# Performance work log

Measured on AMD Instinct MI355X. Metric: run time of the kernel, lower is better.

The kernel has to match this reference:

```python
import jax, jax.numpy as jnp
import numpy as np

B, T = 4096, 256
COND, INTV, H = 128, 64, 256


def _glorot(key, shape):
    fan_in = shape[0]
    return jax.random.normal(key, shape, dtype=jnp.float32) / np.sqrt(fan_in)


def setup_inputs() -> dict:
    key = jax.random.key(0)
    ks = jax.random.split(key, 20)
    inp = {
        "cond": jax.random.normal(ks[0], (B, COND), dtype=jnp.float32),
        "interval_feat": jax.random.normal(ks[1], (B, INTV), dtype=jnp.float32),
        "times": jnp.cumsum(jax.random.uniform(ks[2], (B, T), dtype=jnp.float32), axis=1),
        "seq_lens": jax.random.randint(ks[3], (B,), 1, T + 1),
        # seq_feature MLP: INTV -> 2*INTV -> 2*INTV -> INTV
        "w1": _glorot(ks[4], (INTV, 2 * INTV)), "b1": jnp.zeros((2 * INTV,), jnp.float32),
        "w2": _glorot(ks[5], (2 * INTV, 2 * INTV)), "b2": jnp.zeros((2 * INTV,), jnp.float32),
        "w3": _glorot(ks[6], (2 * INTV, INTV)), "b3": jnp.zeros((INTV,), jnp.float32),
        # h0 projection: (COND+INTV) -> H
        "w_h0": _glorot(ks[7], (COND + INTV, H)), "b_h0": jnp.zeros((H,), jnp.float32),
        # GRUCell (input dim 1), gate order r,z,n
        "w_ih": _glorot(ks[8], (1, 3 * H)), "b_ih": jnp.zeros((3 * H,), jnp.float32),
        "w_hh": _glorot(ks[9], (H, 3 * H)), "b_hh": jnp.zeros((3 * H,), jnp.float32),
        # head: H -> 2 (delta, stop logit)
        "w_head": _glorot(ks[10], (H, 2)), "b_head": jnp.zeros((2,), jnp.float32),
    }
    return inp


def reference(cond, interval_feat, times, seq_lens,
              w1, b1, w2, b2, w3, b3, w_h0, b_h0,
              w_ih, w_hh, b_ih, b_hh, w_head, b_head):
    # seq_feature MLP
    s = jax.nn.relu(interval_feat @ w1 + b1)
    s = jax.nn.relu(s @ w2 + b2)
    seq_emb = s @ w3 + b3
    # initial hidden state
    h0 = jnp.tanh(jnp.concatenate([cond, seq_emb], axis=-1) @ w_h0 + b_h0)  # (B,H)
    # ground-truth deltas; step 0 input is 0, step i>=1 input is gt_delta[:, i-1]
    gt_delta = jnp.diff(times, axis=1, prepend=jnp.zeros((times.shape[0], 1), times.dtype))  # (B,T)
    xs = jnp.concatenate([jnp.zeros((1, times.shape[0]), times.dtype), gt_delta.T], axis=0)  # (T+1,B)

    def step(h, x):
        gi = x[:, None] * w_ih[0] + b_ih          # (B,3H)
        gh = h @ w_hh + b_hh                       # (B,3H)
        gi_r, gi_z, gi_n = jnp.split(gi, 3, axis=-1)
        gh_r, gh_z, gh_n = jnp.split(gh, 3, axis=-1)
        r = jax.nn.sigmoid(gi_r + gh_r)
        z = jax.nn.sigmoid(gi_z + gh_z)
        n = jnp.tanh(gi_n + r * gh_n)
        h_new = (1.0 - z) * n + z * h
        out = h_new @ w_head + b_head              # (B,2)
        return h_new, out

    _, outs = jax.lax.scan(step, h0, xs)           # outs: (T+1,B,2)
    pred_delta = outs[:, :, 0].T                   # (B,T+1)
    stop_logits = outs[:, :, 1].T                  # (B,T+1)
    return pred_delta, stop_logits
```

## Files before the change

kernel.cpp:

```cpp
#include <hip/hip_runtime.h>
#include <cstddef>

typedef _Float16 f16x8 __attribute__((ext_vector_type(8)));
typedef _Float16 f16x2 __attribute__((ext_vector_type(2)));
typedef float    f32x4 __attribute__((ext_vector_type(4)));

#define Bc 4096
#define Tc 256
#define NSTEP 257
#define RB 16
#define HSTR 264
#define GSTR 12
#define HEAD_OFF 393216

__device__ inline float sigm(float x)  { return __builtin_amdgcn_rcpf(1.f + __expf(-x)); }
__device__ inline float tanh_(float x) { return 1.f - 2.f * __builtin_amdgcn_rcpf(1.f + __expf(2.f * x)); }

__global__ __launch_bounds__(256) void build_frags(
    const float* __restrict__ w_hh, const float* __restrict__ w_head,
    _Float16* __restrict__ ws)
{
    int flat = blockIdx.x * 256 + threadIdx.x;
    if (blockIdx.x < 96) {
        int f    = flat >> 6;
        int lane = flat & 63;
        int kt   = f & 7;
        int nc   = (f >> 3) % 3;
        int trio = f / 24;
        int c     = nc * 256 + (trio >> 1) * 32 + 2 * (lane & 15) + (trio & 1);
        int kbase = kt * 32 + (lane >> 4) * 8;
        _Float16* dst = ws + (size_t)f * 512 + (size_t)lane * 8;
        #pragma unroll
        for (int j = 0; j < 8; ++j)
            dst[j] = (_Float16)w_hh[(size_t)(kbase + j) * 768 + c];
    } else {
        int idx = flat - 96 * 256;
        int kt   = idx >> 6;
        int lane = idx & 63;
        int col   = lane & 15;
        int kbase = kt * 32 + (lane >> 4) * 8;
        _Float16* dst = ws + HEAD_OFF / 2 + (size_t)kt * 512 + (size_t)lane * 8;
        #pragma unroll
        for (int j = 0; j < 8; ++j)
            dst[j] = (col < 2) ? (_Float16)w_head[(size_t)(kbase + j) * 2 + col]
                               : (_Float16)0.f;
    }
}

__global__ __attribute__((amdgpu_waves_per_eu(2, 2))) __launch_bounds__(512)
void gru_mfma(
    const float* __restrict__ cond, const float* __restrict__ ivf,
    const float* __restrict__ times,
    const float* __restrict__ w1, const float* __restrict__ b1,
    const float* __restrict__ w2, const float* __restrict__ b2,
    const float* __restrict__ w3, const float* __restrict__ b3,
    const float* __restrict__ wh0, const float* __restrict__ bh0,
    const float* __restrict__ w_ih, const float* __restrict__ b_ih,
    const float* __restrict__ b_hh, const float* __restrict__ b_head,
    const _Float16* __restrict__ wfrag,
    float* __restrict__ out)
{
    __shared__ __align__(16) _Float16 h16[RB * HSTR];
    __shared__ __align__(16) float xs4[4 * NSTEP * 4];
    __shared__ __align__(16) _Float16 headB[4096];
    __shared__ __align__(16) float gateC[256 * GSTR];
    __shared__ float  outbuf[2][2][RB][16];
    __shared__ float  bh2[2];
    __shared__ float  mlp1[RB * 128];
    __shared__ float  mlp2[RB * 128];
    __shared__ float  embS[RB * 64];
    __shared__ float  h0f[RB * 256];

    const int tid  = threadIdx.x;
    const int w    = tid >> 6;
    const int lane = tid & 63;
    const int l15  = lane & 15;
    const int q    = lane >> 4;
    const int row0 = blockIdx.x * RB;

    for (int o = tid; o < RB * 128; o += 512) {
        int r = o >> 7, c = o & 127;
        float a = b1[c];
        #pragma unroll 4
        for (int k = 0; k < 64; ++k)
            a = fmaf(ivf[(size_t)(row0 + r) * 64 + k], w1[k * 128 + c], a);
        mlp1[o] = fmaxf(a, 0.f);
    }
    __syncthreads();
    for (int o = tid; o < RB * 128; o += 512) {
        int r = o >> 7, c = o & 127;
        float a = b2[c];
        #pragma unroll 4
        for (int k = 0; k < 128; ++k)
            a = fmaf(mlp1[r * 128 + k], w2[k * 128 + c], a);
        mlp2[o] = fmaxf(a, 0.f);
    }
    __syncthreads();
    for (int o = tid; o < RB * 64; o += 512) {
        int r = o >> 6, c = o & 63;
        float a = b3[c];
        #pragma unroll 4
        for (int k = 0; k < 128; ++k)
            a = fmaf(mlp2[r * 128 + k], w3[k * 64 + c], a);
        embS[o] = a;
    }
    __syncthreads();
    for (int o = tid; o < RB * 256; o += 512) {
        int r = o >> 8, c = o & 255;
        float a = bh0[c];
        #pragma unroll 4
        for (int k = 0; k < 128; ++k)
            a = fmaf(cond[(size_t)(row0 + r) * 128 + k], wh0[k * 256 + c], a);
        #pragma unroll 4
        for (int k = 0; k < 64; ++k)
            a = fmaf(embS[r * 64 + k], wh0[(128 + k) * 256 + c], a);
        float h = tanh_(a);
        h0f[o] = h;
        h16[r * HSTR + c] = (_Float16)h;
    }

    for (int o = tid; o < 4 * NSTEP; o += 512) {
        int qg = o / NSTEP, ii = o - qg * NSTEP;
        #pragma unroll
        for (int jj = 0; jj < 4; ++jj) {
            int r = qg * 4 + jj;
            float x = 0.f;
            if (ii >= 1) {
                float a = times[(size_t)(row0 + r) * Tc + (ii - 1)];
                float b = (ii >= 2) ? times[(size_t)(row0 + r) * Tc + (ii - 2)] : 0.f;
                x = a - b;
            }
            xs4[o * 4 + jj] = x;
        }
    }
    {
        const float4* src = (const float4*)(wfrag + HEAD_OFF / 2);
        ((float4*)headB)[tid] = src[tid];
    }
    for (int uu = tid; uu < 256; uu += 512) {
        gateC[uu * GSTR + 0] = w_ih[uu];
        gateC[uu * GSTR + 1] = w_ih[256 + uu];
        gateC[uu * GSTR + 2] = w_ih[512 + uu];
        gateC[uu * GSTR + 3] = b_ih[uu] + b_hh[uu];
        gateC[uu * GSTR + 4] = b_ih[256 + uu] + b_hh[256 + uu];
        gateC[uu * GSTR + 5] = b_ih[512 + uu];
        gateC[uu * GSTR + 6] = b_hh[512 + uu];
        gateC[uu * GSTR + 7] = 0.f;
    }
    if (tid < 2) bh2[tid] = b_head[tid];

    const int u0 = w * 32 + 2 * l15;
    const int u1 = u0 + 1;

    f16x8 Bf[2][3][8];
    #pragma unroll
    for (int p = 0; p < 2; ++p)
        #pragma unroll
        for (int nc = 0; nc < 3; ++nc)
            #pragma unroll
            for (int kt = 0; kt < 8; ++kt)
                Bf[p][nc][kt] = *(const f16x8*)(wfrag
                    + (size_t)(((2 * w + p) * 3 + nc) * 8 + kt) * 512
                    + (size_t)lane * 8);

    __syncthreads();

    float hold[2][4];
    #pragma unroll
    for (int p = 0; p < 2; ++p)
        #pragma unroll
        for (int j = 0; j < 4; ++j)
            hold[p][j] = h0f[(q * 4 + j) * 256 + u0 + p];

    for (int i = 0; i <= NSTEP; ++i) {
        const bool doGh = (i < NSTEP);
        const bool doHd = (i >= 1) && (w == 0);

        if (i >= 17 && ((i - 17) & 15) == 0) {
            const int obase = i - 17;
            const int par   = (obase >> 4) & 1;
            const int e     = tid & 15;
            const int row   = (tid >> 4) & 15;
            const int plane = tid >> 8;
            out[(size_t)plane * ((size_t)Bc * NSTEP)
                + (size_t)(row0 + row) * NSTEP + obase + e]
                = outbuf[par][plane][row][e] + bh2[plane];
        }

        f32x4 aR[2], aZ[2], aN[2];
        #pragma unroll
        for (int p = 0; p < 2; ++p) {
            aR[p] = (f32x4){0.f, 0.f, 0.f, 0.f};
            aZ[p] = (f32x4){0.f, 0.f, 0.f, 0.f};
            aN[p] = (f32x4){0.f, 0.f, 0.f, 0.f};
        }
        f32x4 aH = (f32x4){0.f, 0.f, 0.f, 0.f};

        const _Float16* abase = h16 + l15 * HSTR + q * 8;
        #pragma unroll
        for (int kt = 0; kt < 8; ++kt) {
            if (doGh || doHd) {
                f16x8 Af = *(const f16x8*)(abase + kt * 32);
                if (doGh) {
                    #pragma unroll
                    for (int p = 0; p < 2; ++p) {
                        aR[p] = __builtin_amdgcn_mfma_f32_16x16x32_f16(Af, Bf[p][0][kt], aR[p], 0, 0, 0);
                        aZ[p] = __builtin_amdgcn_mfma_f32_16x16x32_f16(Af, Bf[p][1][kt], aZ[p], 0, 0, 0);
                        aN[p] = __builtin_amdgcn_mfma_f32_16x16x32_f16(Af, Bf[p][2][kt], aN[p], 0, 0, 0);
                    }
                }
                if (doHd) {
                    f16x8 Bh = *(const f16x8*)(headB + kt * 512 + lane * 8);
                    aH = __builtin_amdgcn_mfma_f32_16x16x32_f16(Af, Bh, aH, 0, 0, 0);
                }
            }
        }

        if (doHd && l15 < 2) {
            const int o = i - 1;
            #pragma unroll
            for (int j = 0; j < 4; ++j)
                outbuf[(o >> 4) & 1][l15][q * 4 + j][o & 15] = aH[j];
        }

        __syncthreads();

        if (doGh) {
            const f32x4 xv  = *(const f32x4*)(xs4 + (q * NSTEP + i) * 4);
            const f32x4 g0a = *(const f32x4*)(gateC + u0 * GSTR);
            const f32x4 g1a = *(const f32x4*)(gateC + u0 * GSTR + 4);
            const f32x4 g0b = *(const f32x4*)(gateC + u1 * GSTR);
            const f32x4 g1b = *(const f32x4*)(gateC + u1 * GSTR + 4);
            #pragma unroll
            for (int j = 0; j < 4; ++j) {
                const int m = q * 4 + j;
                const float x = xv[j];

                const float rr0 = sigm(fmaf(x, g0a[0], g0a[3]) + aR[0][j]);
                const float zz0 = sigm(fmaf(x, g0a[1], g1a[0]) + aZ[0][j]);
                const float nn0 = tanh_(fmaf(x, g0a[2], g1a[1]) + rr0 * (aN[0][j] + g1a[2]));
                const float h0_ = nn0 + zz0 * (hold[0][j] - nn0);
                hold[0][j] = h0_;

                const float rr1 = sigm(fmaf(x, g0b[0], g0b[3]) + aR[1][j]);
                const float zz1 = sigm(fmaf(x, g0b[1], g1b[0]) + aZ[1][j]);
                const float nn1 = tanh_(fmaf(x, g0b[2], g1b[1]) + rr1 * (aN[1][j] + g1b[2]));
                const float h1_ = nn1 + zz1 * (hold[1][j] - nn1);
                hold[1][j] = h1_;

                *(f16x2*)(h16 + m * HSTR + u0) = (f16x2){(_Float16)h0_, (_Float16)h1_};
            }
        }
        __syncthreads();
    }

    {
        const int e     = tid & 15;
        const int row   = (tid >> 4) & 15;
        const int plane = tid >> 8;
        if (e < 1) {
            out[(size_t)plane * ((size_t)Bc * NSTEP)
                + (size_t)(row0 + row) * NSTEP + 256 + e]
                = outbuf[0][plane][row][e] + bh2[plane];
        }
    }
}

extern "C" void kernel_launch(void* const* d_in, const int* in_sizes, int n_in,
                              void* d_out, int out_size, void* d_ws, size_t ws_size,
                              hipStream_t stream) {
    const float* cond   = (const float*)d_in[0];
    const float* ivf    = (const float*)d_in[1];
    const float* times  = (const float*)d_in[2];
    const float* w1     = (const float*)d_in[4];
    const float* b1     = (const float*)d_in[5];
    const float* w2     = (const float*)d_in[6];
    const float* b2     = (const float*)d_in[7];
    const float* w3     = (const float*)d_in[8];
    const float* b3     = (const float*)d_in[9];
    const float* wh0    = (const float*)d_in[10];
    const float* bh0    = (const float*)d_in[11];
    const float* w_ih   = (const float*)d_in[12];
    const float* b_ih   = (const float*)d_in[13];
    const float* w_hh   = (const float*)d_in[14];
    const float* b_hh   = (const float*)d_in[15];
    const float* w_head = (const float*)d_in[16];
    const float* b_head = (const float*)d_in[17];

    float*    outp = (float*)d_out;
    _Float16* ws   = (_Float16*)d_ws;

    build_frags<<<98, 256, 0, stream>>>(w_hh, w_head, ws);
    gru_mfma<<<Bc / RB, 512, 0, stream>>>(cond, ivf, times,
                                          w1, b1, w2, b2, w3, b3, wh0, bh0,
                                          w_ih, b_ih, b_hh, b_head,
                                          (const _Float16*)ws, outp);
}
```

Before: 705.1 us.

## Double-buffer GRU hidden state to drop one barrier per step, fold log2e into weights

Keeps the fp16 hidden state in two LDS buffers (ping-pong) so each recurrence step needs one __syncthreads instead of two. The fp32 hidden state moves from registers into an LDS array. The log2(e) factors are pre-folded into the recurrent weights and gate constants so the sigmoid and tanh can use a raw exp2. The step loop is also manually unrolled by two to alternate the buffers, and the tail output flush is restructured. The costs are extra LDS traffic for the fp32 state and a slight precision change from scaling the weights before fp16 conversion.

```diff
diff --git a/kernel.cpp b/kernel.cpp
--- a/kernel.cpp
+++ b/kernel.cpp
@@ -10,10 +10,17 @@
 #define NSTEP 257
 #define RB 16
 #define HSTR 264
+#define FSTR 260
 #define GSTR 12
 #define HEAD_OFF 393216
-
-__device__ inline float sigm(float x)  { return __builtin_amdgcn_rcpf(1.f + __expf(-x)); }
+#define LOG2E 1.4426950408889634f
+
+#if __has_builtin(__builtin_amdgcn_exp2f)
+#define EXP2(x) __builtin_amdgcn_exp2f(x)
+#else
+#define EXP2(x) __builtin_exp2f(x)
+#endif
+
 __device__ inline float tanh_(float x) { return 1.f - 2.f * __builtin_amdgcn_rcpf(1.f + __expf(2.f * x)); }
 
 __global__ __launch_bounds__(256) void build_frags(
@@ -27,12 +34,13 @@
         int kt   = f & 7;
         int nc   = (f >> 3) % 3;
         int trio = f / 24;
+        float scale = (nc == 2) ? 2.f * LOG2E : -LOG2E;
         int c     = nc * 256 + (trio >> 1) * 32 + 2 * (lane & 15) + (trio & 1);
         int kbase = kt * 32 + (lane >> 4) * 8;
         _Float16* dst = ws + (size_t)f * 512 + (size_t)lane * 8;
         #pragma unroll
         for (int j = 0; j < 8; ++j)
-            dst[j] = (_Float16)w_hh[(size_t)(kbase + j) * 768 + c];
+            dst[j] = (_Float16)(scale * w_hh[(size_t)(kbase + j) * 768 + c]);
     } else {
         int idx = flat - 96 * 256;
         int kt   = idx >> 6;
@@ -60,7 +68,9 @@
     const _Float16* __restrict__ wfrag,
     float* __restrict__ out)
 {
-    __shared__ __align__(16) _Float16 h16[RB * HSTR];
+    __shared__ __align__(16) _Float16 hA[RB * HSTR];
+    __shared__ __align__(16) _Float16 hB[RB * HSTR];
+    __shared__ __align__(8)  float hF[RB * FSTR];
     __shared__ __align__(16) float xs4[4 * NSTEP * 4];
     __shared__ __align__(16) _Float16 headB[4096];
     __shared__ __align__(16) float gateC[256 * GSTR];
@@ -116,7 +126,7 @@
             a = fmaf(embS[r * 64 + k], wh0[(128 + k) * 256 + c], a);
         float h = tanh_(a);
         h0f[o] = h;
-        h16[r * HSTR + c] = (_Float16)h;
+        hA[r * HSTR + c] = (_Float16)h;
     }
 
     for (int o = tid; o < 4 * NSTEP; o += 512) {
@@ -138,13 +148,13 @@
         ((float4*)headB)[tid] = src[tid];
     }
     for (int uu = tid; uu < 256; uu += 512) {
-        gateC[uu * GSTR + 0] = w_ih[uu];
-        gateC[uu * GSTR + 1] = w_ih[256 + uu];
-        gateC[uu * GSTR + 2] = w_ih[512 + uu];
-        gateC[uu * GSTR + 3] = b_ih[uu] + b_hh[uu];
-        gateC[uu * GSTR + 4] = b_ih[256 + uu] + b_hh[256 + uu];
-        gateC[uu * GSTR + 5] = b_ih[512 + uu];
-        gateC[uu * GSTR + 6] = b_hh[512 + uu];
+        gateC[uu * GSTR + 0] = -LOG2E * w_ih[uu];
+        gateC[uu * GSTR + 1] = -LOG2E * w_ih[256 + uu];
+        gateC[uu * GSTR + 2] = 2.f * LOG2E * w_ih[512 + uu];
+        gateC[uu * GSTR + 3] = -LOG2E * (b_ih[uu] + b_hh[uu]);
+        gateC[uu * GSTR + 4] = -LOG2E * (b_ih[256 + uu] + b_hh[256 + uu]);
+        gateC[uu * GSTR + 5] = 2.f * LOG2E * b_ih[512 + uu];
+        gateC[uu * GSTR + 6] = 2.f * LOG2E * b_hh[512 + uu];
         gateC[uu * GSTR + 7] = 0.f;
     }
     if (tid < 2) bh2[tid] = b_head[tid];
@@ -163,107 +173,171 @@
                     + (size_t)(((2 * w + p) * 3 + nc) * 8 + kt) * 512
                     + (size_t)lane * 8);
 
+    #pragma unroll
+    for (int j = 0; j < 4; ++j) {
+        const int m = q * 4 + j;
+        *(float2*)(hF + m * FSTR + u0) =
+            (float2){h0f[m * 256 + u0], h0f[m * 256 + u1]};
+    }
+
     __syncthreads();
 
-    float hold[2][4];
-    #pragma unroll
-    for (int p = 0; p < 2; ++p)
-        #pragma unroll
-        for (int j = 0; j < 4; ++j)
-            hold[p][j] = h0f[(q * 4 + j) * 256 + u0 + p];
-
-    for (int i = 0; i <= NSTEP; ++i) {
-        const bool doGh = (i < NSTEP);
-        const bool doHd = (i >= 1) && (w == 0);
-
-        if (i >= 17 && ((i - 17) & 15) == 0) {
-            const int obase = i - 17;
-            const int par   = (obase >> 4) & 1;
-            const int e     = tid & 15;
-            const int row   = (tid >> 4) & 15;
-            const int plane = tid >> 8;
-            out[(size_t)plane * ((size_t)Bc * NSTEP)
-                + (size_t)(row0 + row) * NSTEP + obase + e]
-                = outbuf[par][plane][row][e] + bh2[plane];
-        }
-
-        f32x4 aR[2], aZ[2], aN[2];
-        #pragma unroll
-        for (int p = 0; p < 2; ++p) {
-            aR[p] = (f32x4){0.f, 0.f, 0.f, 0.f};
-            aZ[p] = (f32x4){0.f, 0.f, 0.f, 0.f};
-            aN[p] = (f32x4){0.f, 0.f, 0.f, 0.f};
-        }
-        f32x4 aH = (f32x4){0.f, 0.f, 0.f, 0.f};
-
-        const _Float16* abase = h16 + l15 * HSTR + q * 8;
-        #pragma unroll
-        for (int kt = 0; kt < 8; ++kt) {
-            if (doGh || doHd) {
-                f16x8 Af = *(const f16x8*)(abase + kt * 32);
-                if (doGh) {
-                    #pragma unroll
-                    for (int p = 0; p < 2; ++p) {
-                        aR[p] = __builtin_amdgcn_mfma_f32_16x16x32_f16(Af, Bf[p][0][kt], aR[p], 0, 0, 0);
-                        aZ[p] = __builtin_amdgcn_mfma_f32_16x16x32_f16(Af, Bf[p][1][kt], aZ[p], 0, 0, 0);
-                        aN[p] = __builtin_amdgcn_mfma_f32_16x16x32_f16(Af, Bf[p][2][kt], aN[p], 0, 0, 0);
-                    }
-                }
-                if (doHd) {
-                    f16x8 Bh = *(const f16x8*)(headB + kt * 512 + lane * 8);
-                    aH = __builtin_amdgcn_mfma_f32_16x16x32_f16(Af, Bh, aH, 0, 0, 0);
-                }
+    const f32x4 Z4 = (f32x4){0.f, 0.f, 0.f, 0.f};
+
+#define GRU_STEP(HC, HN, I, DOHEAD)                                            \
+do {                                                                           \
+    const int i_ = (I);                                                        \
+    if (i_ >= 17 && ((i_ - 17) & 15) == 0) {                                   \
+        const int obase = i_ - 17;                                             \
+        const int par   = (obase >> 4) & 1;                                    \
+        const int e     = tid & 15;                                            \
+        const int row   = (tid >> 4) & 15;                                     \
+        const int plane = tid >> 8;                                            \
+        out[(size_t)plane * ((size_t)Bc * NSTEP)                               \
+            + (size_t)(row0 + row) * NSTEP + obase + e]                        \
+            = outbuf[par][plane][row][e] + bh2[plane];                         \
+    }                                                                          \
+    f32x4 aR0, aR1, aZ0, aZ1, aN0, aN1, aH = Z4;                               \
+    const _Float16* ab_ = (HC) + l15 * HSTR + q * 8;                           \
+    {                                                                          \
+        f16x8 Af = *(const f16x8*)(ab_);                                       \
+        aR0 = __builtin_amdgcn_mfma_f32_16x16x32_f16(Af, Bf[0][0][0], Z4, 0, 0, 0); \
+        aZ0 = __builtin_amdgcn_mfma_f32_16x16x32_f16(Af, Bf[0][1][0], Z4, 0, 0, 0); \
+        aN0 = __builtin_amdgcn_mfma_f32_16x16x32_f16(Af, Bf[0][2][0], Z4, 0, 0, 0); \
+        aR1 = __builtin_amdgcn_mfma_f32_16x16x32_f16(Af, Bf[1][0][0], Z4, 0, 0, 0); \
+        aZ1 = __builtin_amdgcn_mfma_f32_16x16x32_f16(Af, Bf[1][1][0], Z4, 0, 0, 0); \
+        aN1 = __builtin_amdgcn_mfma_f32_16x16x32_f16(Af, Bf[1][2][0], Z4, 0, 0, 0); \
+        if ((DOHEAD) && w == 0) {                                              \
+            f16x8 Bh = *(const f16x8*)(headB + lane * 8);                      \
+            aH = __builtin_amdgcn_mfma_f32_16x16x32_f16(Af, Bh, Z4, 0, 0, 0);  \
+        }                                                                      \
+    }                                                                          \
+    _Pragma("unroll")                                                          \
+    for (int kt = 1; kt < 8; ++kt) {                                           \
+        f16x8 Af = *(const f16x8*)(ab_ + kt * 32);                             \
+        aR0 = __builtin_amdgcn_mfma_f32_16x16x32_f16(Af, Bf[0][0][kt], aR0, 0, 0, 0); \
+        aZ0 = __builtin_amdgcn_mfma_f32_16x16x32_f16(Af, Bf[0][1][kt], aZ0, 0, 0, 0); \
+        aN0 = __builtin_amdgcn_mfma_f32_16x16x32_f16(Af, Bf[0][2][kt], aN0, 0, 0, 0); \
+        aR1 = __builtin_amdgcn_mfma_f32_16x16x32_f16(Af, Bf[1][0][kt], aR1, 0, 0, 0); \
+        aZ1 = __builtin_amdgcn_mfma_f32_16x16x32_f16(Af, Bf[1][1][kt], aZ1, 0, 0, 0); \
+        aN1 = __builtin_amdgcn_mfma_f32_16x16x32_f16(Af, Bf[1][2][kt], aN1, 0, 0, 0); \
+        if ((DOHEAD) && w == 0) {                                              \
+            f16x8 Bh = *(const f16x8*)(headB + kt * 512 + lane * 8);           \
+            aH = __builtin_amdgcn_mfma_f32_16x16x32_f16(Af, Bh, aH, 0, 0, 0);  \
+        }                                                                      \
+    }                                                                          \
+    if ((DOHEAD) && w == 0 && l15 < 2) {                                       \
+        const int o = i_ - 1;                                                  \
+        _Pragma("unroll")                                                      \
+        for (int j = 0; j < 4; ++j)                                            \
+            outbuf[(o >> 4) & 1][l15][q * 4 + j][o & 15] = aH[j];              \
+    }                                                                          \
+                              \
+    {                                                                          \
+        float xr[4];                                                           \
+        _Pragma("unroll")                                                      \
+        for (int j = 0; j < 4; ++j) xr[j] = xs4[(q * NSTEP + i_) * 4 + j];     \
+        float h0n[4], hoy[4];                                                  \
+        {                                               \
+            const f32x4 g0 = *(const f32x4*)(gateC + u0 * GSTR);               \
+            const f32x4 g1 = *(const f32x4*)(gateC + u0 * GSTR + 4);           \
+            float sr[4], sz[4], pn[4], ab[4], rr[4], zz[4], nn[4];             \
+            _Pragma("unroll")                                                  \
+            for (int j = 0; j < 4; ++j) {                                      \
+                sr[j] = fmaf(xr[j], g0[0], g0[3]) + aR0[j];                    \
+                sz[j] = fmaf(xr[j], g0[1], g1[0]) + aZ0[j];                    \
+                pn[j] = fmaf(xr[j], g0[2], g1[1]);                             \
+                ab[j] = aN0[j] + g1[2];                                        \
+            }                                                                  \
+            _Pragma("unroll")                                                  \
+            for (int j = 0; j < 4; ++j)                                        \
+                rr[j] = __builtin_amdgcn_rcpf(1.f + EXP2(sr[j]));              \
+            _Pragma("unroll")                                                  \
+            for (int j = 0; j < 4; ++j)                                        \
+                zz[j] = __builtin_amdgcn_rcpf(1.f + EXP2(sz[j]));              \
+            _Pragma("unroll")                                                  \
+            for (int j = 0; j < 4; ++j) {                                      \
+                float sn = fmaf(rr[j], ab[j], pn[j]);                          \
+                nn[j] = fmaf(-2.f, __builtin_amdgcn_rcpf(1.f + EXP2(sn)), 1.f);\
+            }                                                                  \
+            _Pragma("unroll")                                                  \
+            for (int j = 0; j < 4; ++j) {                                      \
+                const int m = q * 4 + j;                                       \
+                float2 ho = *(float2*)(hF + m * FSTR + u0);                    \
+                h0n[j] = nn[j] + zz[j] * (ho.x - nn[j]);                       \
+                hoy[j] = ho.y;                                                 \
+            }                                                                  \
+        }                                                                      \
+        {                                                \
+            const f32x4 g0 = *(const f32x4*)(gateC + u1 * GSTR);               \
+            const f32x4 g1 = *(const f32x4*)(gateC + u1 * GSTR + 4);           \
+            float sr[4], sz[4], pn[4], ab[4], rr[4], zz[4], nn[4];             \
+            _Pragma("unroll")                                                  \
+            for (int j = 0; j < 4; ++j) {                                      \
+                sr[j] = fmaf(xr[j], g0[0], g0[3]) + aR1[j];                    \
+                sz[j] = fmaf(xr[j], g0[1], g1[0]) + aZ1[j];                    \
+                pn[j] = fmaf(xr[j], g0[2], g1[1]);                             \
+                ab[j] = aN1[j] + g1[2];                                        \
+            }                                                                  \
+            _Pragma("unroll")                                                  \
+            for (int j = 0; j < 4; ++j)                                        \
+                rr[j] = __builtin_amdgcn_rcpf(1.f + EXP2(sr[j]));              \
+            _Pragma("unroll")                                                  \
+            for (int j = 0; j < 4; ++j)                                        \
+                zz[j] = __builtin_amdgcn_rcpf(1.f + EXP2(sz[j]));              \
+            _Pragma("unroll")                                                  \
+            for (int j = 0; j < 4; ++j) {                                      \
+                float sn = fmaf(rr[j], ab[j], pn[j]);                          \
+                nn[j] = fmaf(-2.f, __builtin_amdgcn_rcpf(1.f + EXP2(sn)), 1.f);\
+            }                                                                  \
+            _Pragma("unroll")                                                  \
+            for (int j = 0; j < 4; ++j) {                                      \
+                const int m = q * 4 + j;                                       \
+                float h1n = nn[j] + zz[j] * (hoy[j] - nn[j]);                  \
+                *(float2*)(hF + m * FSTR + u0) = (float2){h0n[j], h1n};        \
+                *(f16x2*)((HN) + m * HSTR + u0) =                              \
+                    (f16x2){(_Float16)h0n[j], (_Float16)h1n};                  \
+            }                                                                  \
+        }                                                                      \
+    }                                                                          \
+    __syncthreads();                                                           \
+} while (0)
+
+    GRU_STEP(hA, hB, 0, false);
+    for (int i = 1; i < 256; i += 2) {
+        GRU_STEP(hB, hA, i, true);
+        GRU_STEP(hA, hB, i + 1, true);
+    }
+
+    {
+        if (w == 0) {
+            f32x4 aH = Z4;
+            const _Float16* ab_ = hB + l15 * HSTR + q * 8;
+            #pragma unroll
+            for (int kt = 0; kt < 8; ++kt) {
+                f16x8 Af = *(const f16x8*)(ab_ + kt * 32);
+                f16x8 Bh = *(const f16x8*)(headB + kt * 512 + lane * 8);
+                aH = __builtin_amdgcn_mfma_f32_16x16x32_f16(Af, Bh, aH, 0, 0, 0);
             }
-        }
-
-        if (doHd && l15 < 2) {
-            const int o = i - 1;
-            #pragma unroll
-            for (int j = 0; j < 4; ++j)
-                outbuf[(o >> 4) & 1][l15][q * 4 + j][o & 15] = aH[j];
-        }
-
-        __syncthreads();
-
-        if (doGh) {
-            const f32x4 xv  = *(const f32x4*)(xs4 + (q * NSTEP + i) * 4);
-            const f32x4 g0a = *(const f32x4*)(gateC + u0 * GSTR);
-            const f32x4 g1a = *(const f32x4*)(gateC + u0 * GSTR + 4);
-            const f32x4 g0b = *(const f32x4*)(gateC + u1 * GSTR);
-            const f32x4 g1b = *(const f32x4*)(gateC + u1 * GSTR + 4);
-            #pragma unroll
-            for (int j = 0; j < 4; ++j) {
-                const int m = q * 4 + j;
-                const float x = xv[j];
-
-                const float rr0 = sigm(fmaf(x, g0a[0], g0a[3]) + aR[0][j]);
-                const float zz0 = sigm(fmaf(x, g0a[1], g1a[0]) + aZ[0][j]);
-                const float nn0 = tanh_(fmaf(x, g0a[2], g1a[1]) + rr0 * (aN[0][j] + g1a[2]));
-                const float h0_ = nn0 + zz0 * (hold[0][j] - nn0);
-                hold[0][j] = h0_;
-
-                const float rr1 = sigm(fmaf(x, g0b[0], g0b[3]) + aR[1][j]);
-                const float zz1 = sigm(fmaf(x, g0b[1], g1b[0]) + aZ[1][j]);
-                const float nn1 = tanh_(fmaf(x, g0b[2], g1b[1]) + rr1 * (aN[1][j] + g1b[2]));
-                const float h1_ = nn1 + zz1 * (hold[1][j] - nn1);
-                hold[1][j] = h1_;
-
-                *(f16x2*)(h16 + m * HSTR + u0) = (f16x2){(_Float16)h0_, (_Float16)h1_};
+            if (l15 < 2) {
+                #pragma unroll
+                for (int j = 0; j < 4; ++j)
+                    outbuf[0][l15][q * 4 + j][0] = aH[j];
             }
         }
         __syncthreads();
-    }
-
-    {
         const int e     = tid & 15;
         const int row   = (tid >> 4) & 15;
         const int plane = tid >> 8;
-        if (e < 1) {
+        out[(size_t)plane * ((size_t)Bc * NSTEP)
+            + (size_t)(row0 + row) * NSTEP + 240 + e]
+            = outbuf[1][plane][row][e] + bh2[plane];
+        if (e == 0)
             out[(size_t)plane * ((size_t)Bc * NSTEP)
-                + (size_t)(row0 + row) * NSTEP + 256 + e]
-                = outbuf[0][plane][row][e] + bh2[plane];
-        }
-    }
+                + (size_t)(row0 + row) * NSTEP + 256]
+                = outbuf[0][plane][row][0] + bh2[plane];
+    }
+#undef GRU_STEP
 }
 
 extern "C" void kernel_launch(void* const* d_in, const int* in_sizes, int n_in,
```

Result: no change. 711.8 us (+0.9%).
